# Kernel optimization log

Measured on AMD Instinct MI355X. Metric: run time of the kernel, lower is better.

The kernel has to match this reference:

```python
import jax, jax.numpy as jnp
import numpy as np

D_MODEL = 1024
ED = 2048          # d_inner = 2 * d_model
N = 16             # d_state
DT_RANK = 64
K = 4              # d_conv
BETA = 0.6
ALPHA = 1.0
B_SZ, L = 1, 2048


def setup_inputs() -> dict:
    key = jax.random.key(0)
    ks = jax.random.split(key, 9)
    s = 0.02
    x = jax.random.normal(ks[0], (B_SZ, L, D_MODEL), jnp.float32)
    W_in = jax.random.normal(ks[1], (2 * ED, D_MODEL), jnp.float32) * s
    conv_w = jax.random.normal(ks[2], (ED, K), jnp.float32) * s
    conv_b = jax.random.normal(ks[3], (ED,), jnp.float32) * s
    W_x = jax.random.normal(ks[4], (DT_RANK + 2 * N, ED), jnp.float32) * s
    dt_std = DT_RANK ** -0.5
    W_dt = jax.random.uniform(ks[5], (ED, DT_RANK), jnp.float32, -dt_std, dt_std)
    # dt bias init: inverse-softplus of dt in [dt_min, dt_max]
    dt = jnp.exp(jax.random.uniform(ks[6], (ED,), jnp.float32)
                 * (np.log(0.1) - np.log(0.001)) + np.log(0.001))
    dt = jnp.clip(dt, 1e-4)
    b_dt = dt + jnp.log(-jnp.expm1(-dt))
    A_log = jnp.log(jnp.tile(jnp.arange(1, N + 1, dtype=jnp.float32), (ED, 1)))
    D = jnp.ones((ED,), jnp.float32)
    W_out = jax.random.normal(ks[7], (D_MODEL, ED), jnp.float32) * s
    return {"x": x, "W_in": W_in, "conv_w": conv_w, "conv_b": conv_b,
            "W_x": W_x, "W_dt": W_dt, "b_dt": b_dt, "A_log": A_log,
            "D": D, "W_out": W_out}


def _depthwise_causal_conv(xc, conv_w, conv_b):
    # xc: (B, L, ED); torch Conv1d(groups=ED, padding=K-1)[..., :L] == causal conv
    lhs = jnp.transpose(xc, (0, 2, 1))                       # (B, ED, L)
    lhs = jnp.pad(lhs, ((0, 0), (0, 0), (K - 1, 0)))
    out = jax.lax.conv_general_dilated(lhs, conv_w[:, None, :], (1,), 'VALID',
                                       feature_group_count=ED)  # (B, ED, L)
    return jnp.transpose(out, (0, 2, 1)) + conv_b


def _ssm_momentum(xc, W_x, W_dt, b_dt, A_log, D):
    A = -jnp.exp(A_log)                                      # (ED, N)
    dBC = xc @ W_x.T                                         # (B, L, dt_rank + 2N)
    delta, Bm, Cm = jnp.split(dBC, [DT_RANK, DT_RANK + N], axis=-1)
    delta = jax.nn.softplus(delta @ W_dt.T + b_dt)           # (B, L, ED)
    deltaA = jnp.exp(delta[..., None] * A)                   # (B, L, ED, N)
    u = ALPHA * delta[..., None] * Bm[:, :, None, :] * xc[..., None]  # (B, L, ED, N)

    def step(carry, inp):
        h, v = carry
        dA_t, u_t = inp
        v = BETA * v + u_t
        h = dA_t * h + v
        return (h, v), h

    h0 = jnp.zeros((xc.shape[0], ED, N), xc.dtype)
    _, hs = jax.lax.scan(step, (h0, h0),
                         (jnp.moveaxis(deltaA, 1, 0), jnp.moveaxis(u, 1, 0)))
    y = jnp.einsum('lben,bln->ble', hs, Cm)                  # (B, L, ED)
    return y + D * xc


def reference(x, W_in, conv_w, conv_b, W_x, W_dt, b_dt, A_log, D, W_out):
    xz = x @ W_in.T                                          # (B, L, 2*ED)
    xc, z = jnp.split(xz, 2, axis=-1)
    xc = jax.nn.silu(_depthwise_causal_conv(xc, conv_w, conv_b))
    y = _ssm_momentum(xc, W_x, W_dt, b_dt, A_log, D)
    return (y * jax.nn.silu(z)) @ W_out.T                    # (B, L, d_model)
```

## Files before the change

kernel.cpp:

```cpp
#include <hip/hip_runtime.h>
#include <hip/hip_bf16.h>
#include <math.h>

#define L 2048
#define DM 1024
#define ED 2048
#define NST 16
#define DTR 64
#define BETA 0.6f
#define NCHUNK 64
#define LCH 32
#define SPLITS 16
#define SPLIT4 4

typedef __bf16 bf16_t;
typedef __bf16 bf16x8 __attribute__((ext_vector_type(8)));
typedef __bf16 bf16x4 __attribute__((ext_vector_type(4)));
typedef __bf16 bf16x2 __attribute__((ext_vector_type(2)));
typedef float  floatx4 __attribute__((ext_vector_type(4)));


__global__ void k_fill(float* __restrict__ p, float v, int n) {
    int i = blockIdx.x * 256 + threadIdx.x;
    if (i < n) p[i] = v;
}

__global__ void k_cvt_all(const float4* __restrict__ s0, bf16x4* __restrict__ d0,
                          const float4* __restrict__ s1, bf16x4* __restrict__ d1,
                          const float4* __restrict__ s2, bf16x4* __restrict__ d2,
                          const float4* __restrict__ s3, bf16x4* __restrict__ d3,
                          const float4* __restrict__ s4, bf16x4* __restrict__ d4) {
    int i = blockIdx.x * 256 + threadIdx.x;
    const float4* s; bf16x4* d; int j;
    if (i < 524288)        { s = s0; d = d0; j = i; }
    else if (i < 1572864)  { s = s1; d = d1; j = i - 524288; }
    else if (i < 1622016)  { s = s2; d = d2; j = i - 1572864; }
    else if (i < 1654784)  { s = s3; d = d3; j = i - 1622016; }
    else                   { s = s4; d = d4; j = i - 1654784; }
    float4 f = s[j];
    bf16x4 o;
    o[0] = (bf16_t)f.x; o[1] = (bf16_t)f.y; o[2] = (bf16_t)f.z; o[3] = (bf16_t)f.w;
    d[j] = o;
}

template<int EPI, bool GUARD>
__global__ __launch_bounds__(256)
void k_gemm_bt(const bf16_t* __restrict__ X, const bf16_t* __restrict__ W,
               float* __restrict__ C, int M, int N, int K, int ldc, int ksz,
               const float* __restrict__ bias) {
    __shared__ bf16_t As[128 * 32];
    __shared__ bf16_t Bs[128 * 32];
    const int tid  = threadIdx.x;
    const int bx   = blockIdx.x, by = blockIdx.y;
    const int kbase = blockIdx.z * ksz;
    const size_t zoff = (size_t)blockIdx.z * M * ldc;
    const int wave = tid >> 6, lane = tid & 63;
    const int wm   = (wave >> 1) * 64;
    const int wn   = (wave & 1) * 64;
    const int quad = lane >> 4, l16 = lane & 15;

    floatx4 acc[4][4];
#pragma unroll
    for (int i = 0; i < 4; i++)
#pragma unroll
        for (int j = 0; j < 4; j++)
            acc[i][j] = (floatx4){0.f, 0.f, 0.f, 0.f};

    for (int kt = kbase; kt < kbase + ksz; kt += 32) {
        if (GUARD) {
#pragma unroll
            for (int p = 0; p < 2; p++) {
                int e = p * 2048 + tid * 8;
                int r = e >> 5, c = e & 31;
                int arow = by * 128 + r;
                *(float4*)(&As[r * 32 + c]) =
                    *(const float4*)(&X[(size_t)arow * K + kt + c]);
                int brow = bx * 128 + r;
                float4 bv = make_float4(0.f, 0.f, 0.f, 0.f);
                if (brow < N) bv = *(const float4*)(&W[(size_t)brow * K + kt + c]);
                *(float4*)(&Bs[r * 32 + c]) = bv;
            }
        } else {
#pragma unroll
            for (int p = 0; p < 2; p++) {
                int e = p * 2048 + tid * 8;
                int r = e >> 5, c = e & 31;
                __builtin_amdgcn_global_load_lds(
                    (const __attribute__((address_space(1))) void*)&X[(size_t)(by * 128 + r) * K + kt + c],
                    (__attribute__((address_space(3))) void*)&As[e], 16, 0, 0);
                __builtin_amdgcn_global_load_lds(
                    (const __attribute__((address_space(1))) void*)&W[(size_t)(bx * 128 + r) * K + kt + c],
                    (__attribute__((address_space(3))) void*)&Bs[e], 16, 0, 0);
            }
        }
        __syncthreads();

        bf16x8 af[4], bfr[4];
#pragma unroll
        for (int mt = 0; mt < 4; mt++)
            af[mt] = *(const bf16x8*)(&As[(wm + mt * 16 + l16) * 32 + quad * 8]);
#pragma unroll
        for (int nt = 0; nt < 4; nt++)
            bfr[nt] = *(const bf16x8*)(&Bs[(wn + nt * 16 + l16) * 32 + quad * 8]);
#pragma unroll
        for (int mt = 0; mt < 4; mt++)
#pragma unroll
            for (int nt = 0; nt < 4; nt++)
                acc[mt][nt] = __builtin_amdgcn_mfma_f32_16x16x32_bf16(
                    af[mt], bfr[nt], acc[mt][nt], 0, 0, 0);
        __syncthreads();
    }

#pragma unroll
    for (int mt = 0; mt < 4; mt++) {
#pragma unroll
        for (int nt = 0; nt < 4; nt++) {
            int col = bx * 128 + wn + nt * 16 + l16;
            if (!GUARD || col < N) {
#pragma unroll
                for (int r4 = 0; r4 < 4; r4++) {
                    int row = by * 128 + wm + mt * 16 + quad * 4 + r4;
                    float v = acc[mt][nt][r4];
                    size_t off = zoff + (size_t)row * ldc + col;
                    if (EPI == 0) {
                        C[off] = v;
                    } else if (EPI == 1) {
                        v += bias[col];
                        v = (v > 20.f) ? v : __logf(1.f + __expf(v));
                        ((bf16_t*)C)[off] = (bf16_t)v;
                    } else {
                        ((bf16_t*)C)[off] = (bf16_t)v;
                    }
                }
            }
        }
    }
}

__global__ void k_red4(const bf16x8* __restrict__ part, float4* __restrict__ out) {
    int i = blockIdx.x * 256 + threadIdx.x;
    const int stride = L * DM / 8;
    bf16x8 a = part[i], b = part[i + stride];
    bf16x8 c = part[i + 2 * stride], d = part[i + 3 * stride];
    float4 o0, o1;
    o0.x = (float)a[0] + (float)b[0] + (float)c[0] + (float)d[0];
    o0.y = (float)a[1] + (float)b[1] + (float)c[1] + (float)d[1];
    o0.z = (float)a[2] + (float)b[2] + (float)c[2] + (float)d[2];
    o0.w = (float)a[3] + (float)b[3] + (float)c[3] + (float)d[3];
    o1.x = (float)a[4] + (float)b[4] + (float)c[4] + (float)d[4];
    o1.y = (float)a[5] + (float)b[5] + (float)c[5] + (float)d[5];
    o1.z = (float)a[6] + (float)b[6] + (float)c[6] + (float)d[6];
    o1.w = (float)a[7] + (float)b[7] + (float)c[7] + (float)d[7];
    out[2 * i]     = o0;
    out[2 * i + 1] = o1;
}

__global__ void k_conv_silu(const bf16_t* __restrict__ xz,
                            const float* __restrict__ conv_w,
                            const float* __restrict__ conv_b,
                            bf16_t* __restrict__ xc_bf) {
    int idx = blockIdx.x * 256 + threadIdx.x;
    int t  = idx >> 8;
    int e8 = (idx & 255) * 8;
    float4 w[8];
#pragma unroll
    for (int j = 0; j < 8; j++) w[j] = *(const float4*)(&conv_w[(e8 + j) * 4]);
    float acc[8];
#pragma unroll
    for (int j = 0; j < 8; j++) acc[j] = conv_b[e8 + j];
#pragma unroll
    for (int k = 0; k < 4; k++) {
        int tt = t - (3 - k);
        if (tt >= 0) {
            bf16x8 v = *(const bf16x8*)(xz + (size_t)tt * 4096 + e8);
#pragma unroll
            for (int j = 0; j < 8; j++)
                acc[j] += ((const float*)&w[j])[k] * (float)v[j];
        }
    }
    bf16x8 o;
#pragma unroll
    for (int j = 0; j < 8; j++) {
        float s = acc[j] / (1.f + __expf(-acc[j]));
        o[j] = (bf16_t)s;
    }
    *(bf16x8*)(xc_bf + (size_t)t * ED + e8) = o;
}

__global__ void k_red2(const float* __restrict__ part, float* __restrict__ dBC,
                       bf16_t* __restrict__ dly) {
    int idx = blockIdx.x * 256 + threadIdx.x;
    int t = idx / 96, c = idx - t * 96;
    float s = 0.f;
#pragma unroll
    for (int sp = 0; sp < SPLITS; sp++) s += part[(size_t)sp * L * 96 + idx];
    dBC[idx] = s;
    if (c < 64) dly[t * 64 + c] = (bf16_t)s;
}


__global__ __launch_bounds__(256)
void k_scan_p1(const bf16_t* __restrict__ delta, const bf16_t* __restrict__ xc,
               const float* __restrict__ dBC, const float* __restrict__ A_log,
               float2* __restrict__ hv, bf16x2* __restrict__ pq) {
    const int chunk = blockIdx.x >> 3;
    const int e = (blockIdx.x & 7) * 256 + threadIdx.x;
    float A[NST];
#pragma unroll
    for (int n = 0; n < NST; n++) A[n] = -__expf(A_log[e * NST + n]);
    float h[NST], v[NST], p[NST], q[NST];
#pragma unroll
    for (int n = 0; n < NST; n++) { h[n] = 0.f; v[n] = 0.f; p[n] = 1.f; q[n] = 0.f; }
    float bp = 1.f;
    const int t0 = chunk * LCH;
    for (int i = 0; i < LCH; i++) {
        int t = t0 + i;
        float d   = (float)delta[(size_t)t * ED + e];
        float xcv = (float)xc[(size_t)t * ED + e];
        float du  = d * xcv;
        bp *= BETA;
        const float* Bp = &dBC[t * 96 + 64];
#pragma unroll
        for (int n = 0; n < NST; n++) {
            float a = __expf(d * A[n]);
            v[n] = BETA * v[n] + du * Bp[n];
            h[n] = a * h[n] + v[n];
            p[n] *= a;
            q[n] = a * q[n] + bp;
        }
    }
#pragma unroll
    for (int n = 0; n < NST; n++) {
        size_t idx = ((size_t)n * NCHUNK + chunk) * ED + e;
        hv[idx] = make_float2(h[n], v[n]);
        bf16x2 z; z[0] = (bf16_t)p[n]; z[1] = (bf16_t)q[n];
        pq[idx] = z;
    }
}

__global__ void k_combine(float2* __restrict__ hv, const bf16x2* __restrict__ pq) {
    int tid = blockIdx.x * 256 + threadIdx.x;
    int n = tid >> 11, e = tid & (ED - 1);
    float h = 0.f, v = 0.f;
    const float bl = 7.9586611e-8f;
#pragma unroll 4
    for (int c = 0; c < NCHUNK; c++) {
        size_t idx = ((size_t)n * NCHUNK + c) * ED + e;
        float2 f = hv[idx];
        bf16x2 z = pq[idx];
        hv[idx] = make_float2(h, v);
        float hn = (float)z[0] * h + (float)z[1] * v + f.x;
        v = bl * v + f.y;
        h = hn;
    }
}

__global__ __launch_bounds__(256)
void k_scan_p2(const bf16_t* __restrict__ delta, const bf16_t* __restrict__ xc,
               const float* __restrict__ dBC, const float* __restrict__ A_log,
               const float2* __restrict__ hv, const float* __restrict__ Dvec,
               const bf16_t* __restrict__ xz, bf16_t* __restrict__ g) {
    const int chunk = blockIdx.x >> 3;
    const int e = (blockIdx.x & 7) * 256 + threadIdx.x;
    float A[NST];
#pragma unroll
    for (int n = 0; n < NST; n++) A[n] = -__expf(A_log[e * NST + n]);
    float h[NST], v[NST];
#pragma unroll
    for (int n = 0; n < NST; n++) {
        float2 s = hv[((size_t)n * NCHUNK + chunk) * ED + e];
        h[n] = s.x; v[n] = s.y;
    }
    const float De = Dvec[e];
    const int t0 = chunk * LCH;
    for (int i = 0; i < LCH; i++) {
        int t = t0 + i;
        float d   = (float)delta[(size_t)t * ED + e];
        float xcv = (float)xc[(size_t)t * ED + e];
        float du  = d * xcv;
        const float* Bp = &dBC[t * 96 + 64];
        const float* Cp = &dBC[t * 96 + 80];
        float yacc = 0.f;
#pragma unroll
        for (int n = 0; n < NST; n++) {
            float a = __expf(d * A[n]);
            v[n] = BETA * v[n] + du * Bp[n];
            h[n] = a * h[n] + v[n];
            yacc += Cp[n] * h[n];
        }
        float z = (float)xz[(size_t)t * 4096 + ED + e];
        float sz = z / (1.f + __expf(-z));
        g[(size_t)t * ED + e] = (bf16_t)((yacc + De * xcv) * sz);
    }
}


extern "C" void kernel_launch(void* const* d_in, const int* in_sizes, int n_in,
                              void* d_out, int out_size, void* d_ws, size_t ws_size,
                              hipStream_t stream) {
    const float* x      = (const float*)d_in[0];
    const float* W_in   = (const float*)d_in[1];
    const float* conv_w = (const float*)d_in[2];
    const float* conv_b = (const float*)d_in[3];
    const float* W_x    = (const float*)d_in[4];
    const float* W_dt   = (const float*)d_in[5];
    const float* b_dt   = (const float*)d_in[6];
    const float* A_log  = (const float*)d_in[7];
    const float* Dv     = (const float*)d_in[8];
    const float* W_out  = (const float*)d_in[9];
    float* out = (float*)d_out;

    constexpr size_t OFF_XZ    = 0;
    constexpr size_t OFF_XC    = 33554432;
    constexpr size_t OFF_C     = 50331648;
    constexpr size_t OFF_DELTA = 58720256;
    constexpr size_t OFF_R1    = 75497472;
    constexpr size_t OFF_XBF   = 109051904;
    constexpr size_t OFF_DBC   = 113246208;
    constexpr size_t OFF_DLY   = 114032640;
    constexpr size_t OFF_WX    = 114294784;
    constexpr size_t OFF_WDT   = 114688000;
    constexpr size_t OFF_WOUT  = 114950144;
    constexpr size_t WS_NEED   = 119144448;

    if (ws_size < WS_NEED) {
        k_fill<<<(out_size + 255) / 256, 256, 0, stream>>>(out, 1.0e9f, out_size);
        return;
    }

    char* ws = (char*)d_ws;
    bf16_t* xz_bf = (bf16_t*)(ws + OFF_XZ);
    bf16_t* part4 = (bf16_t*)(ws + OFF_XZ);
    float2* hv    = (float2*)(ws + OFF_XC);
    bf16_t* xc_bf = (bf16_t*)(ws + OFF_C);
    bf16_t* delta_bf = (bf16_t*)(ws + OFF_DELTA);
    bf16_t* g_bf  = (bf16_t*)(ws + OFF_DELTA + 8388608);
    bf16_t* Win_bf  = (bf16_t*)(ws + OFF_R1);
    float*  part2   = (float*)(ws + OFF_R1 + 16777216);
    bf16x2* pq      = (bf16x2*)(ws + OFF_R1);
    bf16_t* x_bf  = (bf16_t*)(ws + OFF_XBF);
    float*  dBC   = (float*)(ws + OFF_DBC);
    bf16_t* dly   = (bf16_t*)(ws + OFF_DLY);
    bf16_t* Wx_bf  = (bf16_t*)(ws + OFF_WX);
    bf16_t* Wdt_bf = (bf16_t*)(ws + OFF_WDT);
    bf16_t* Wout_bf = (bf16_t*)(ws + OFF_WOUT);

    k_cvt_all<<<8512, 256, 0, stream>>>(
        (const float4*)x,     (bf16x4*)x_bf,
        (const float4*)W_in,  (bf16x4*)Win_bf,
        (const float4*)W_x,   (bf16x4*)Wx_bf,
        (const float4*)W_dt,  (bf16x4*)Wdt_bf,
        (const float4*)W_out, (bf16x4*)Wout_bf);

    {
        dim3 g(4096 / 128, L / 128, 1);
        k_gemm_bt<2, false><<<g, 256, 0, stream>>>(
            x_bf, Win_bf, (float*)xz_bf, L, 4096, DM, 4096, DM, nullptr);
    }
    k_conv_silu<<<L * ED / 8 / 256, 256, 0, stream>>>(xz_bf, conv_w, conv_b, xc_bf);
    {
        dim3 g(1, L / 128, SPLITS);
        k_gemm_bt<0, true><<<g, 256, 0, stream>>>(
            xc_bf, Wx_bf, part2, L, 96, ED, 96, ED / SPLITS, nullptr);
    }
    k_red2<<<L * 96 / 256, 256, 0, stream>>>(part2, dBC, dly);
    {
        dim3 g(ED / 128, L / 128, 1);
        k_gemm_bt<1, false><<<g, 256, 0, stream>>>(
            dly, Wdt_bf, (float*)delta_bf, L, ED, DTR, ED, DTR, b_dt);
    }
    k_scan_p1<<<NCHUNK * 8, 256, 0, stream>>>(delta_bf, xc_bf, dBC, A_log, hv, pq);
    k_combine<<<ED * NST / 256, 256, 0, stream>>>(hv, pq);
    k_scan_p2<<<NCHUNK * 8, 256, 0, stream>>>(delta_bf, xc_bf, dBC, A_log, hv, Dv, xz_bf, g_bf);
    {
        dim3 g(DM / 128, L / 128, SPLIT4);
        k_gemm_bt<2, false><<<g, 256, 0, stream>>>(
            g_bf, Wout_bf, (float*)part4, L, DM, ED, DM, ED / SPLIT4, nullptr);
    }
    k_red4<<<L * DM / 8 / 256, 256, 0, stream>>>((const bf16x8*)part4, (float4*)out);
}
```

Before: 248.5 us.

## Fuse causal conv+SiLU into x_proj GEMM loader and both scan passes

Removes the standalone conv+SiLU kernel and the materialized xc buffer. The x_proj GEMM (GUARD path) now computes the 4-tap causal conv and SiLU on the fly while loading its A tile from xz. Both scan passes recompute xc per timestep with a sliding register window over xz. This saves a launch and a write/read of an L×ED bf16 buffer, but repeats the conv and exp work three times and does strided 4096-stride reads in the scans.

```diff
diff --git a/kernel.cpp b/kernel.cpp
--- a/kernel.cpp
+++ b/kernel.cpp
@@ -45,9 +45,11 @@
 
 template<int EPI, bool GUARD>
 __global__ __launch_bounds__(256)
-void k_gemm_bt(const bf16_t* __restrict__ X, const bf16_t* __restrict__ W,
+void k_gemm_bt(const bf16_t* __restrict__ X, int lda,
+               const bf16_t* __restrict__ W,
                float* __restrict__ C, int M, int N, int K, int ldc, int ksz,
-               const float* __restrict__ bias) {
+               const float* __restrict__ bias,
+               const float* __restrict__ cw, const float* __restrict__ cb) {
     __shared__ bf16_t As[128 * 32];
     __shared__ bf16_t Bs[128 * 32];
     const int tid  = threadIdx.x;
@@ -72,9 +74,32 @@
             for (int p = 0; p < 2; p++) {
                 int e = p * 2048 + tid * 8;
                 int r = e >> 5, c = e & 31;
-                int arow = by * 128 + r;
-                *(float4*)(&As[r * 32 + c]) =
-                    *(const float4*)(&X[(size_t)arow * K + kt + c]);
+                int t   = by * 128 + r;
+                int col = kt + c;
+                float accv[8];
+#pragma unroll
+                for (int j = 0; j < 8; j++) accv[j] = cb[col + j];
+                float4 wj[8];
+#pragma unroll
+                for (int j = 0; j < 8; j++)
+                    wj[j] = *(const float4*)(&cw[(col + j) * 4]);
+#pragma unroll
+                for (int k = 0; k < 4; k++) {
+                    int tt = t - 3 + k;
+                    if (tt >= 0) {
+                        bf16x8 xv = *(const bf16x8*)(&X[(size_t)tt * lda + col]);
+#pragma unroll
+                        for (int j = 0; j < 8; j++)
+                            accv[j] += ((const float*)&wj[j])[k] * (float)xv[j];
+                    }
+                }
+                bf16x8 av;
+#pragma unroll
+                for (int j = 0; j < 8; j++) {
+                    float s = accv[j] / (1.f + __expf(-accv[j]));
+                    av[j] = (bf16_t)s;
+                }
+                *(bf16x8*)(&As[r * 32 + c]) = av;
                 int brow = bx * 128 + r;
                 float4 bv = make_float4(0.f, 0.f, 0.f, 0.f);
                 if (brow < N) bv = *(const float4*)(&W[(size_t)brow * K + kt + c]);
@@ -86,7 +111,7 @@
                 int e = p * 2048 + tid * 8;
                 int r = e >> 5, c = e & 31;
                 __builtin_amdgcn_global_load_lds(
-                    (const __attribute__((address_space(1))) void*)&X[(size_t)(by * 128 + r) * K + kt + c],
+                    (const __attribute__((address_space(1))) void*)&X[(size_t)(by * 128 + r) * lda + kt + c],
                     (__attribute__((address_space(3))) void*)&As[e], 16, 0, 0);
                 __builtin_amdgcn_global_load_lds(
                     (const __attribute__((address_space(1))) void*)&W[(size_t)(bx * 128 + r) * K + kt + c],
@@ -155,38 +180,6 @@
     out[2 * i + 1] = o1;
 }
 
-__global__ void k_conv_silu(const bf16_t* __restrict__ xz,
-                            const float* __restrict__ conv_w,
-                            const float* __restrict__ conv_b,
-                            bf16_t* __restrict__ xc_bf) {
-    int idx = blockIdx.x * 256 + threadIdx.x;
-    int t  = idx >> 8;
-    int e8 = (idx & 255) * 8;
-    float4 w[8];
-#pragma unroll
-    for (int j = 0; j < 8; j++) w[j] = *(const float4*)(&conv_w[(e8 + j) * 4]);
-    float acc[8];
-#pragma unroll
-    for (int j = 0; j < 8; j++) acc[j] = conv_b[e8 + j];
-#pragma unroll
-    for (int k = 0; k < 4; k++) {
-        int tt = t - (3 - k);
-        if (tt >= 0) {
-            bf16x8 v = *(const bf16x8*)(xz + (size_t)tt * 4096 + e8);
-#pragma unroll
-            for (int j = 0; j < 8; j++)
-                acc[j] += ((const float*)&w[j])[k] * (float)v[j];
-        }
-    }
-    bf16x8 o;
-#pragma unroll
-    for (int j = 0; j < 8; j++) {
-        float s = acc[j] / (1.f + __expf(-acc[j]));
-        o[j] = (bf16_t)s;
-    }
-    *(bf16x8*)(xc_bf + (size_t)t * ED + e8) = o;
-}
-
 __global__ void k_red2(const float* __restrict__ part, float* __restrict__ dBC,
                        bf16_t* __restrict__ dly) {
     int idx = blockIdx.x * 256 + threadIdx.x;
@@ -200,7 +193,8 @@
 
 
 __global__ __launch_bounds__(256)
-void k_scan_p1(const bf16_t* __restrict__ delta, const bf16_t* __restrict__ xc,
+void k_scan_p1(const bf16_t* __restrict__ delta, const bf16_t* __restrict__ xz,
+               const float* __restrict__ conv_w, const float* __restrict__ conv_b,
                const float* __restrict__ dBC, const float* __restrict__ A_log,
                float2* __restrict__ hv, bf16x2* __restrict__ pq) {
     const int chunk = blockIdx.x >> 3;
@@ -213,10 +207,19 @@
     for (int n = 0; n < NST; n++) { h[n] = 0.f; v[n] = 0.f; p[n] = 1.f; q[n] = 0.f; }
     float bp = 1.f;
     const int t0 = chunk * LCH;
+    const bf16_t* xzx = xz + e;
+    const float4 wv = *(const float4*)(&conv_w[e * 4]);
+    const float cbv = conv_b[e];
+    float x0 = (t0 >= 3) ? (float)xzx[(size_t)(t0 - 3) * 4096] : 0.f;
+    float x1 = (t0 >= 2) ? (float)xzx[(size_t)(t0 - 2) * 4096] : 0.f;
+    float x2 = (t0 >= 1) ? (float)xzx[(size_t)(t0 - 1) * 4096] : 0.f;
     for (int i = 0; i < LCH; i++) {
         int t = t0 + i;
+        float x3 = (float)xzx[(size_t)t * 4096];
+        float a4 = cbv + wv.x * x0 + wv.y * x1 + wv.z * x2 + wv.w * x3;
+        float xcv = a4 / (1.f + __expf(-a4));
+        x0 = x1; x1 = x2; x2 = x3;
         float d   = (float)delta[(size_t)t * ED + e];
-        float xcv = (float)xc[(size_t)t * ED + e];
         float du  = d * xcv;
         bp *= BETA;
         const float* Bp = &dBC[t * 96 + 64];
@@ -256,10 +259,11 @@
 }
 
 __global__ __launch_bounds__(256)
-void k_scan_p2(const bf16_t* __restrict__ delta, const bf16_t* __restrict__ xc,
+void k_scan_p2(const bf16_t* __restrict__ delta, const bf16_t* __restrict__ xz,
+               const float* __restrict__ conv_w, const float* __restrict__ conv_b,
                const float* __restrict__ dBC, const float* __restrict__ A_log,
                const float2* __restrict__ hv, const float* __restrict__ Dvec,
-               const bf16_t* __restrict__ xz, bf16_t* __restrict__ g) {
+               bf16_t* __restrict__ g) {
     const int chunk = blockIdx.x >> 3;
     const int e = (blockIdx.x & 7) * 256 + threadIdx.x;
     float A[NST];
@@ -273,10 +277,19 @@
     }
     const float De = Dvec[e];
     const int t0 = chunk * LCH;
+    const bf16_t* xzx = xz + e;
+    const float4 wv = *(const float4*)(&conv_w[e * 4]);
+    const float cbv = conv_b[e];
+    float x0 = (t0 >= 3) ? (float)xzx[(size_t)(t0 - 3) * 4096] : 0.f;
+    float x1 = (t0 >= 2) ? (float)xzx[(size_t)(t0 - 2) * 4096] : 0.f;
+    float x2 = (t0 >= 1) ? (float)xzx[(size_t)(t0 - 1) * 4096] : 0.f;
     for (int i = 0; i < LCH; i++) {
         int t = t0 + i;
+        float x3 = (float)xzx[(size_t)t * 4096];
+        float a4 = cbv + wv.x * x0 + wv.y * x1 + wv.z * x2 + wv.w * x3;
+        float xcv = a4 / (1.f + __expf(-a4));
+        x0 = x1; x1 = x2; x2 = x3;
         float d   = (float)delta[(size_t)t * ED + e];
-        float xcv = (float)xc[(size_t)t * ED + e];
         float du  = d * xcv;
         const float* Bp = &dBC[t * 96 + 64];
         const float* Cp = &dBC[t * 96 + 80];
@@ -332,7 +345,6 @@
     bf16_t* xz_bf = (bf16_t*)(ws + OFF_XZ);
     bf16_t* part4 = (bf16_t*)(ws + OFF_XZ);
     float2* hv    = (float2*)(ws + OFF_XC);
-    bf16_t* xc_bf = (bf16_t*)(ws + OFF_C);
     bf16_t* delta_bf = (bf16_t*)(ws + OFF_DELTA);
     bf16_t* g_bf  = (bf16_t*)(ws + OFF_DELTA + 8388608);
     bf16_t* Win_bf  = (bf16_t*)(ws + OFF_R1);
@@ -355,27 +367,32 @@
     {
         dim3 g(4096 / 128, L / 128, 1);
         k_gemm_bt<2, false><<<g, 256, 0, stream>>>(
-            x_bf, Win_bf, (float*)xz_bf, L, 4096, DM, 4096, DM, nullptr);
-    }
-    k_conv_silu<<<L * ED / 8 / 256, 256, 0, stream>>>(xz_bf, conv_w, conv_b, xc_bf);
+            x_bf, DM, Win_bf, (float*)xz_bf, L, 4096, DM, 4096, DM,
+            nullptr, nullptr, nullptr);
+    }
     {
         dim3 g(1, L / 128, SPLITS);
         k_gemm_bt<0, true><<<g, 256, 0, stream>>>(
-            xc_bf, Wx_bf, part2, L, 96, ED, 96, ED / SPLITS, nullptr);
+            xz_bf, 4096, Wx_bf, part2, L, 96, ED, 96, ED / SPLITS,
+            nullptr, conv_w, conv_b);
     }
     k_red2<<<L * 96 / 256, 256, 0, stream>>>(part2, dBC, dly);
     {
         dim3 g(ED / 128, L / 128, 1);
         k_gemm_bt<1, false><<<g, 256, 0, stream>>>(
-            dly, Wdt_bf, (float*)delta_bf, L, ED, DTR, ED, DTR, b_dt);
-    }
-    k_scan_p1<<<NCHUNK * 8, 256, 0, stream>>>(delta_bf, xc_bf, dBC, A_log, hv, pq);
+            dly, DTR, Wdt_bf, (float*)delta_bf, L, ED, DTR, ED, DTR,
+            b_dt, nullptr, nullptr);
+    }
+    k_scan_p1<<<NCHUNK * 8, 256, 0, stream>>>(delta_bf, xz_bf, conv_w, conv_b,
+                                              dBC, A_log, hv, pq);
     k_combine<<<ED * NST / 256, 256, 0, stream>>>(hv, pq);
-    k_scan_p2<<<NCHUNK * 8, 256, 0, stream>>>(delta_bf, xc_bf, dBC, A_log, hv, Dv, xz_bf, g_bf);
+    k_scan_p2<<<NCHUNK * 8, 256, 0, stream>>>(delta_bf, xz_bf, conv_w, conv_b,
+                                              dBC, A_log, hv, Dv, g_bf);
     {
         dim3 g(DM / 128, L / 128, SPLIT4);
         k_gemm_bt<2, false><<<g, 256, 0, stream>>>(
-            g_bf, Wout_bf, (float*)part4, L, DM, ED, DM, ED / SPLIT4, nullptr);
+            g_bf, ED, Wout_bf, (float*)part4, L, DM, ED, DM, ED / SPLIT4,
+            nullptr, nullptr, nullptr);
     }
     k_red4<<<L * DM / 8 / 256, 256, 0, stream>>>((const bf16x8*)part4, (float4*)out);
 }
```

Measured after the change: 251.0 us. Within noise of the previous version (+1.0%).
